# Kernel optimization log

Measured on AMD Instinct MI355X. Metric: run time of the kernel, lower is better.

The kernel has to match this reference:

```python
import jax, jax.numpy as jnp
import numpy as np

# irreps_in  = 128x0 + 64x1   (128 scalars, 64 vectors) -> dim 320
# irreps_out = 128x0 + 64x1 ; irreps_with_gates = (128+64)x0 + 64x1
B = 8192          # batch (nodes)
N0, N1 = 128, 64  # input multiplicities: scalars, vectors
NS, NV = 128, 64  # output scalars, gated vectors (NV gates appended to scalars)

_eps = np.zeros((3, 3, 3), np.float32)
_eps[0, 1, 2] = _eps[1, 2, 0] = _eps[2, 0, 1] = 1.0
_eps[0, 2, 1] = _eps[2, 1, 0] = _eps[1, 0, 2] = -1.0
EPS = jnp.asarray(_eps)  # Levi-Civita, used for the 1x1->1 CG path


def setup_inputs() -> dict:
    key = jax.random.key(0)
    ks = jax.random.split(key, 5)
    x = jax.random.normal(ks[0], (B, N0 + 3 * N1), jnp.float32)
    # fully-connected (uvw) path weights of the tensor square
    w000 = jax.random.normal(ks[1], (N0, N0, NS + NV), jnp.float32)
    w110 = jax.random.normal(ks[2], (N1, N1, NS + NV), jnp.float32)
    w011 = jax.random.normal(ks[3], (N0, N1, NV), jnp.float32)
    w111 = jax.random.normal(ks[4], (N1, N1, NV), jnp.float32)
    return {"x": x, "w000": w000, "w110": w110, "w011": w011, "w111": w111}


def reference(x, w000, w110, w011, w111):
    x0 = x[:, :N0]                        # [B, N0] scalars
    x1 = x[:, N0:].reshape(-1, N1, 3)     # [B, N1, 3] vectors

    inv_sqrt2 = 1.0 / np.sqrt(2.0)

    # ---- tensor square, scalar (l=0) outputs: NS scalars + NV gates ----
    s000 = jnp.einsum('bu,bv,uvw->bw', x0, x0, w000) * (1.0 / N0)
    dots = jnp.einsum('bui,bvi->buv', x1, x1) * (1.0 / np.sqrt(3.0))
    s110 = jnp.einsum('buv,uvw->bw', dots, w110) * (1.0 / N1)
    scalars = (s000 + s110) * inv_sqrt2   # [B, NS+NV], avg over 2 paths

    # ---- tensor square, vector (l=1) outputs: NV vectors ----
    v011 = jnp.einsum('bu,bvi,uvw->bwi', x0, x1, w011) * (1.0 / np.sqrt(N0 * N1))
    v111 = jnp.einsum('ijk,bui,bvj,uvw->bwk', EPS, x1, x1, w111) * (inv_sqrt2 / N1)
    vecs = (v011 + v111) * inv_sqrt2      # [B, NV, 3]

    # ---- e3nn.nn.Gate ----
    s_out = jax.nn.silu(scalars[:, :NS])            # act_scalars on true scalars
    g = jax.nn.sigmoid(scalars[:, NS:])             # act_gates on NV gate scalars
    v_out = vecs * g[:, :, None]                    # gate the non-scalar irreps

    return jnp.concatenate([s_out, v_out.reshape(v_out.shape[0], -1)], axis=1)
```

## Files before the change

### kernel.cpp

```cpp
#include <hip/hip_runtime.h>
#include <cstdint>

static constexpr int B_  = 8192;
static constexpr int NW_ = 192;

typedef __attribute__((ext_vector_type(8))) _Float16 h8v;
typedef __attribute__((ext_vector_type(2))) _Float16 h2v;
typedef __attribute__((ext_vector_type(4))) float f4v;
typedef __attribute__((ext_vector_type(2))) float f2v;
typedef __attribute__((ext_vector_type(4))) unsigned u4v;
typedef __attribute__((ext_vector_type(2))) unsigned u2v;

#define DI __device__ __forceinline__

DI h2v uh(unsigned u) { return __builtin_bit_cast(h2v, u); }
DI unsigned hu(h2v h) { return __builtin_bit_cast(unsigned, h); }
DI h2v hsplat(unsigned short bits) {
  _Float16 v = __builtin_bit_cast(_Float16, bits);
  h2v t; t.x = v; t.y = v; return t;
}
DI unsigned hpack(float lo, float hi) {
  h2v t; t.x = (_Float16)lo; t.y = (_Float16)hi;
  return __builtin_bit_cast(unsigned, t);
}
DI short f2h_bits(float f) { return __builtin_bit_cast(short, (_Float16)f); }

DI f4v mfma16h(h8v a, h8v b, f4v c) {
  return __builtin_amdgcn_mfma_f32_16x16x32_f16(a, b, c, 0, 0, 0);
}

static constexpr unsigned PK_BU0 = 606436u;
static constexpr unsigned PK_BV0 = 1030628u;
static constexpr unsigned PK_BU2 = 4u;
static constexpr unsigned PK_BV2 = 20u;
DI int tab2(unsigned pack, int blk) { return (int)((pack >> (2 * blk)) & 3u); }

__global__ void prep_all(const float* __restrict__ w000, const float* __restrict__ w110,
                         const float* __restrict__ w011, const float* __restrict__ w111,
                         short* __restrict__ wsc, short* __restrict__ wve) {
  __shared__ unsigned short T[32][200];
  const int t = threadIdx.x;
  const int bi = blockIdx.x;
  const float s000 = 1.0f / (128.0f * 1.41421356237f);
  const float s110 = 1.0f / (64.0f * 2.44948974968f);
  const float sv   = 1.0f / 128.0f;

  if (bi < 416) {
    const int s = bi;
    const float* W; int dim; float scale; int blk, ik, bu, bv;
    if (s < 320) {
      blk = s >> 5; ik = s & 31;
      bu = tab2(PK_BU0, blk); bv = tab2(PK_BV0, blk);
      W = w000; dim = 128; scale = s000;
    } else {
      int sp = s - 320; blk = sp >> 5; ik = sp & 31;
      bu = tab2(PK_BU2, blk); bv = tab2(PK_BV2, blk);
      W = w110; dim = 64; scale = s110;
    }
    const int u = bu * 32 + ik;
    const int v = t >> 3, l8 = t & 7;
    float a[24];
    const float* pA = W + ((size_t)(u * dim) + bv * 32 + v) * 192 + l8 * 24;
#pragma unroll
    for (int jj = 0; jj < 6; ++jj) {
      f4v x4 = *(const f4v*)(pA + jj * 4);
      a[jj * 4] = x4.x; a[jj * 4 + 1] = x4.y; a[jj * 4 + 2] = x4.z; a[jj * 4 + 3] = x4.w;
    }
    if (bu != bv) {
      const float* pB = W + ((size_t)((bv * 32 + v)) * dim + u) * 192 + l8 * 24;
#pragma unroll
      for (int jj = 0; jj < 6; ++jj) {
        f4v x4 = *(const f4v*)(pB + jj * 4);
        a[jj * 4] += x4.x; a[jj * 4 + 1] += x4.y; a[jj * 4 + 2] += x4.z; a[jj * 4 + 3] += x4.w;
      }
    }
    unsigned o[12];
#pragma unroll
    for (int i = 0; i < 12; ++i) o[i] = hpack(a[2 * i] * scale, a[2 * i + 1] * scale);
#pragma unroll
    for (int i = 0; i < 3; ++i)
      *(u4v*)(&T[v][l8 * 24 + i * 8]) = u4v{o[4 * i], o[4 * i + 1], o[4 * i + 2], o[4 * i + 3]};
    __syncthreads();
    short* dst = wsc + (size_t)s * 6144;
#pragma unroll
    for (int k = 0; k < 3; ++k) {
      const int unit = t * 3 + k;
      const int F = unit >> 6, lane = unit & 63;
      const int n = F * 16 + (lane & 15);
      const int vr = (lane >> 4) * 8;
      short oo[8];
#pragma unroll
      for (int j = 0; j < 8; ++j) oo[j] = (short)T[vr + j][n];
      *(h8v*)(dst + F * 512 + lane * 8) = *(h8v*)oo;
    }
  } else {
    const int s = bi - 416;
    if (s < 256) {
      const int k32 = t >> 3, l8 = t & 7;
      const float* p = w011 + ((size_t)(s * 32 + k32)) * 64 + l8 * 8;
      f4v x0_ = *(const f4v*)p, x1_ = *(const f4v*)(p + 4);
      u4v o{hpack(x0_.x * sv, x0_.y * sv), hpack(x0_.z * sv, x0_.w * sv),
            hpack(x1_.x * sv, x1_.y * sv), hpack(x1_.z * sv, x1_.w * sv)};
      *(u4v*)(&T[k32][l8 * 8]) = o;
    } else {
      const int sp = s - 256;
      const int blk = sp >> 5, ik = sp & 31;
      const int bu = tab2(PK_BU2, blk), bv = tab2(PK_BV2, blk);
      const int u = bu * 32 + ik;
      const int v = t >> 3, l8 = t & 7;
      float a[8];
      const float* pA = w111 + ((size_t)(u * 64) + bv * 32 + v) * 64 + l8 * 8;
      f4v x0_ = *(const f4v*)pA, x1_ = *(const f4v*)(pA + 4);
      a[0] = x0_.x; a[1] = x0_.y; a[2] = x0_.z; a[3] = x0_.w;
      a[4] = x1_.x; a[5] = x1_.y; a[6] = x1_.z; a[7] = x1_.w;
      if (bu != bv) {
        const float* pB = w111 + ((size_t)((bv * 32 + v)) * 64 + u) * 64 + l8 * 8;
        f4v y0 = *(const f4v*)pB, y1 = *(const f4v*)(pB + 4);
        a[0] -= y0.x; a[1] -= y0.y; a[2] -= y0.z; a[3] -= y0.w;
        a[4] -= y1.x; a[5] -= y1.y; a[6] -= y1.z; a[7] -= y1.w;
      }
      u4v o{hpack(a[0] * sv, a[1] * sv), hpack(a[2] * sv, a[3] * sv),
            hpack(a[4] * sv, a[5] * sv), hpack(a[6] * sv, a[7] * sv)};
      *(u4v*)(&T[v][l8 * 8]) = o;
    }
    __syncthreads();
    const int nf = t >> 6, lane = t & 63;
    const int n = nf * 16 + (lane & 15);
    const int vr = (lane >> 4) * 8;
    short oo[8];
#pragma unroll
    for (int j = 0; j < 8; ++j) oo[j] = (short)T[vr + j][n];
    *(h8v*)(wve + (size_t)s * 2048 + nf * 512 + lane * 8) = *(h8v*)oo;
  }
}

#define X0H_STRIDE 136
#define X1_STRIDE  200

DI void stage_x64w(const float* __restrict__ x, int b0,
                   unsigned short* X0H, unsigned short* X1) {
  const int t = threadIdx.x;
#pragma unroll
  for (int pass = 0; pass < 2; ++pass) {
    const int row = pass * 32 + (t >> 4), l16 = t & 15;
    const float* src = x + (size_t)(b0 + row) * 320;
    f4v v0 = *(const f4v*)(src + l16 * 8);
    f4v v1 = *(const f4v*)(src + l16 * 8 + 4);
    u4v o{hpack(v0.x, v0.y), hpack(v0.z, v0.w), hpack(v1.x, v1.y), hpack(v1.z, v1.w)};
    *(u4v*)(&X0H[row * X0H_STRIDE + l16 * 8]) = o;
    float buf[12];
    f4v a0 = *(const f4v*)(src + 128 + l16 * 12);
    f4v a1 = *(const f4v*)(src + 128 + l16 * 12 + 4);
    f4v a2 = *(const f4v*)(src + 128 + l16 * 12 + 8);
    buf[0] = a0.x; buf[1] = a0.y; buf[2] = a0.z; buf[3] = a0.w;
    buf[4] = a1.x; buf[5] = a1.y; buf[6] = a1.z; buf[7] = a1.w;
    buf[8] = a2.x; buf[9] = a2.y; buf[10] = a2.z; buf[11] = a2.w;
#pragma unroll
    for (int i = 0; i < 3; ++i) {
      u2v w2{hpack(buf[i], buf[3 + i]), hpack(buf[6 + i], buf[9 + i])};
      *(u2v*)(&X1[row * X1_STRIDE + i * 64 + l16 * 4]) = w2;
    }
  }
}

DI void loadB6(h8v* dst, const short* __restrict__ p) {
#pragma unroll
  for (int nf = 0; nf < 6; ++nf) dst[nf] = *(const h8v*)(p + nf * 512);
}
DI void loadB2(h8v* dst, const short* __restrict__ p) {
  dst[0] = *(const h8v*)p;
  dst[1] = *(const h8v*)(p + 512);
}

__global__ __launch_bounds__(512, 2)
void gemm_split(const float* __restrict__ x, const short* __restrict__ wsc,
                const short* __restrict__ wve,
                float* __restrict__ Psc, float* __restrict__ Pve) {
  __shared__ unsigned short X0H[64 * X0H_STRIDE];
  __shared__ unsigned short X1[64 * X1_STRIDE];
  const int xcd = blockIdx.x & 7;
  const int kb  = xcd >> 2;
  const int tile = (blockIdx.x >> 3) * 4 + (xcd & 3);
  const int b0 = tile * 64;

  stage_x64w(x, b0, X0H, X1);
  __syncthreads();

  const int t0 = threadIdx.x;
  const int w = t0 >> 6, lane = t0 & 63;
  const bool isvec = w >= 4;
  const int nh = w & 1, mr = (w >> 1) & 1;
  const int q = lane >> 4, r = lane & 15, q8 = q * 8;

  f4v acc[12];
#pragma unroll
  for (int i = 0; i < 12; ++i) acc[i] = f4v{0.f, 0.f, 0.f, 0.f};

  if (!isvec) {
    const unsigned short* x0f[2];
    const unsigned short* x1f[2];
#pragma unroll
    for (int f = 0; f < 2; ++f) {
      x0f[f] = &X0H[(mr * 32 + f * 16 + r) * X0H_STRIDE];
      x1f[f] = &X1[(mr * 32 + f * 16 + r) * X1_STRIDE];
    }

    {
      const int s0 = kb * 160;
      const short* wp = wsc + ((size_t)s0 * 12 + nh * 6) * 512 + lane * 8;
      u4v pv[2]; pv[0] = u4v{0, 0, 0, 0}; pv[1] = u4v{0, 0, 0, 0};
      int bu32 = 0;
      h8v b[4][6];
      loadB6(b[0], wp); loadB6(b[1], wp + 6144); loadB6(b[2], wp + 12288);
      for (int t4 = 0; t4 < 40; ++t4) {
#pragma unroll
        for (int uu = 0; uu < 4; ++uu) {
          const int t = t4 * 4 + uu;
          if (t < 157) loadB6(b[(uu + 3) & 3], wp + (size_t)(t + 3) * 6144);
          const int s = s0 + t;
          const int ik = s & 31;
          if (t == 0 || ik == 0) {
            const int blk = s >> 5;
            const int bv32 = tab2(PK_BV0, blk) * 32;
            bu32 = tab2(PK_BU0, blk) * 32;
            pv[0] = *(const u4v*)(x0f[0] + bv32 + q8);
            pv[1] = *(const u4v*)(x0f[1] + bv32 + q8);
          }
          h8v a[2];
#pragma unroll
          for (int f = 0; f < 2; ++f) {
            h2v xu = hsplat(x0f[f][bu32 + ik]);
            u4v pa;
#pragma unroll
            for (int m = 0; m < 4; ++m) pa[m] = hu(uh(pv[f][m]) * xu);
            a[f] = __builtin_bit_cast(h8v, pa);
          }
          __builtin_amdgcn_s_setprio(1);
#pragma unroll
          for (int nf = 0; nf < 6; ++nf)
#pragma unroll
            for (int f = 0; f < 2; ++f)
              acc[f * 6 + nf] = mfma16h(a[f], b[uu & 3][nf], acc[f * 6 + nf]);
          __builtin_amdgcn_s_setprio(0);
        }
      }
    }

    {
      const int sp0 = kb * 48;
      const short* wp = wsc + ((size_t)(320 + sp0) * 12 + nh * 6) * 512 + lane * 8;
      h8v b[4][6];
      loadB6(b[0], wp); loadB6(b[1], wp + 6144); loadB6(b[2], wp + 12288);
      for (int t4 = 0; t4 < 12; ++t4) {
#pragma unroll
        for (int uu = 0; uu < 4; ++uu) {
          const int t = t4 * 4 + uu;
          if (t < 45) loadB6(b[(uu + 3) & 3], wp + (size_t)(t + 3) * 6144);
          const int sp = sp0 + t;
          const int blk = sp >> 5, ik = sp & 31;
          const int bu32 = tab2(PK_BU2, blk) * 32;
          const int bv32 = tab2(PK_BV2, blk) * 32;
          h8v a[2];
#pragma unroll
          for (int f = 0; f < 2; ++f) {
            h2v us0 = hsplat(x1f[f][bu32 + ik]);
            h2v us1 = hsplat(x1f[f][64 + bu32 + ik]);
            h2v us2 = hsplat(x1f[f][128 + bu32 + ik]);
            u4v p0 = *(const u4v*)(x1f[f] + bv32 + q8);
            u4v p1 = *(const u4v*)(x1f[f] + 64 + bv32 + q8);
            u4v p2 = *(const u4v*)(x1f[f] + 128 + bv32 + q8);
            u4v pa;
#pragma unroll
            for (int m = 0; m < 4; ++m) {
              h2v sm = uh(p0[m]) * us0;
              sm = sm + uh(p1[m]) * us1;
              sm = sm + uh(p2[m]) * us2;
              pa[m] = hu(sm);
            }
            a[f] = __builtin_bit_cast(h8v, pa);
          }
          __builtin_amdgcn_s_setprio(1);
#pragma unroll
          for (int nf = 0; nf < 6; ++nf)
#pragma unroll
            for (int f = 0; f < 2; ++f)
              acc[f * 6 + nf] = mfma16h(a[f], b[uu & 3][nf], acc[f * 6 + nf]);
          __builtin_amdgcn_s_setprio(0);
        }
      }
    }

#pragma unroll
    for (int f = 0; f < 2; ++f)
#pragma unroll
      for (int nf = 0; nf < 6; ++nf) {
        const int n = (nh * 6 + nf) * 16 + r;
#pragma unroll
        for (int reg = 0; reg < 4; ++reg) {
          const int row = b0 + mr * 32 + f * 16 + q * 4 + reg;
          Psc[((size_t)kb * B_ + row) * NW_ + n] = acc[f * 6 + nf][reg];
        }
      }
  } else {
    const unsigned short* x0r[2];
    const unsigned short* x1r[2];
#pragma unroll
    for (int ff = 0; ff < 2; ++ff) {
      x0r[ff] = &X0H[(mr * 32 + ff * 16 + r) * X0H_STRIDE];
      x1r[ff] = &X1[(mr * 32 + ff * 16 + r) * X1_STRIDE];
    }

    {
      const int u0 = kb * 64;
      const short* wp = wve + (size_t)(u0 * 2) * 2048 + nh * 1024 + lane * 8;
      h8v b[4][2];
      loadB2(b[0], wp); loadB2(b[1], wp + 2048); loadB2(b[2], wp + 4096);
      for (int t4 = 0; t4 < 32; ++t4) {
#pragma unroll
        for (int uu = 0; uu < 4; ++uu) {
          const int t = t4 * 4 + uu;
          if (t < 125) loadB2(b[(uu + 3) & 3], wp + (size_t)(t + 3) * 2048);
          const int g = t >> 1, j = t & 1;
          const int vb = j * 32 + q8;
          h8v a[2][3];
#pragma unroll
          for (int ff = 0; ff < 2; ++ff) {
            h2v xu2 = hsplat(x0r[ff][u0 + g]);
#pragma unroll
            for (int i = 0; i < 3; ++i) {
              u4v p = *(const u4v*)(x1r[ff] + i * 64 + vb);
              u4v pa;
#pragma unroll
              for (int m = 0; m < 4; ++m) pa[m] = hu(uh(p[m]) * xu2);
              a[ff][i] = __builtin_bit_cast(h8v, pa);
            }
          }
          __builtin_amdgcn_s_setprio(1);
#pragma unroll
          for (int ip = 0; ip < 3; ++ip)
#pragma unroll
            for (int nfl = 0; nfl < 2; ++nfl)
#pragma unroll
              for (int ff = 0; ff < 2; ++ff)
                acc[(ff * 3 + ip) * 2 + nfl] =
                    mfma16h(a[ff][ip], b[uu & 3][nfl], acc[(ff * 3 + ip) * 2 + nfl]);
          __builtin_amdgcn_s_setprio(0);
        }
      }
    }

    {
      const int sp0 = kb * 48;
      const short* wp = wve + (size_t)(256 + sp0) * 2048 + nh * 1024 + lane * 8;
      h8v b[4][2];
      loadB2(b[0], wp); loadB2(b[1], wp + 2048); loadB2(b[2], wp + 4096);
      for (int t4 = 0; t4 < 12; ++t4) {
#pragma unroll
        for (int uu = 0; uu < 4; ++uu) {
          const int t = t4 * 4 + uu;
          if (t < 45) loadB2(b[(uu + 3) & 3], wp + (size_t)(t + 3) * 2048);
          const int sp = sp0 + t;
          const int blk = sp >> 5, ik = sp & 31;
          const int bu32 = tab2(PK_BU2, blk) * 32;
          const int bv32 = tab2(PK_BV2, blk) * 32;
          h8v a[2][3];
#pragma unroll
          for (int ff = 0; ff < 2; ++ff) {
            h2v us[3];
            u4v p[3];
#pragma unroll
            for (int i = 0; i < 3; ++i) {
              us[i] = hsplat(x1r[ff][i * 64 + bu32 + ik]);
              p[i] = *(const u4v*)(x1r[ff] + i * 64 + bv32 + q8);
            }
#pragma unroll
            for (int ip = 0; ip < 3; ++ip) {
              const int i1 = (ip + 1) % 3, i2 = (ip + 2) % 3;
              u4v pa;
#pragma unroll
              for (int m = 0; m < 4; ++m)
                pa[m] = hu(uh(p[i2][m]) * us[i1] - uh(p[i1][m]) * us[i2]);
              a[ff][ip] = __builtin_bit_cast(h8v, pa);
            }
          }
          __builtin_amdgcn_s_setprio(1);
#pragma unroll
          for (int ip = 0; ip < 3; ++ip)
#pragma unroll
            for (int nfl = 0; nfl < 2; ++nfl)
#pragma unroll
              for (int ff = 0; ff < 2; ++ff)
                acc[(ff * 3 + ip) * 2 + nfl] =
                    mfma16h(a[ff][ip], b[uu & 3][nfl], acc[(ff * 3 + ip) * 2 + nfl]);
          __builtin_amdgcn_s_setprio(0);
        }
      }
    }

#pragma unroll
    for (int ff = 0; ff < 2; ++ff)
#pragma unroll
      for (int ip = 0; ip < 3; ++ip)
#pragma unroll
        for (int nfl = 0; nfl < 2; ++nfl) {
          const int ai = (ff * 3 + ip) * 2 + nfl;
          const int n = (nh * 2 + nfl) * 16 + r;
#pragma unroll
          for (int reg = 0; reg < 4; ++reg) {
            const int row = b0 + mr * 32 + ff * 16 + q * 4 + reg;
            Pve[(((size_t)kb * 3 + ip) * B_ + row) * 64 + n] = acc[ai][reg];
          }
        }
  }
}

__global__ void reduce_ep(const float* __restrict__ Psc, const float* __restrict__ Pve,
                          float* __restrict__ out) {
  int t = blockIdx.x * blockDim.x + threadIdx.x;
  int b = t / NW_, c = t % NW_;
  float v = Psc[(size_t)b * NW_ + c] + Psc[(size_t)(B_ + b) * NW_ + c];
  float sg = 1.0f / (1.0f + __expf(-v));
  if (c < 128) {
    out[(size_t)b * 320 + c] = v * sg;
  } else {
    int w = c - 128;
#pragma unroll
    for (int i = 0; i < 3; ++i) {
      float vv = Pve[((size_t)i * B_ + b) * 64 + w] +
                 Pve[((size_t)(3 + i) * B_ + b) * 64 + w];
      out[(size_t)b * 320 + 128 + w * 3 + i] = vv * sg;
    }
  }
}

extern "C" void kernel_launch(void* const* d_in, const int* in_sizes, int n_in,
                              void* d_out, int out_size, void* d_ws, size_t ws_size,
                              hipStream_t stream) {
  const float* x    = (const float*)d_in[0];
  const float* w000 = (const float*)d_in[1];
  const float* w110 = (const float*)d_in[2];
  const float* w011 = (const float*)d_in[3];
  const float* w111 = (const float*)d_in[4];
  float* out = (float*)d_out;

  char* ws = (char*)d_ws;
  short* wsc = (short*)ws;
  short* wve = (short*)(ws + 5111808);
  float* Psc = (float*)(ws + 6553600);
  float* Pve = (float*)(ws + 19136512);

  prep_all  <<<768, 256, 0, stream>>>(w000, w110, w011, w111, wsc, wve);
  gemm_split<<<256, 512, 0, stream>>>(x, wsc, wve, Psc, Pve);
  reduce_ep <<<6144, 256, 0, stream>>>(Psc, Pve, out);
}
```

Before: 159.5 us.

## Split K across wave pairs with full M tile per wave, reduce via LDS

Each wave now covers all 64 rows of the tile and half of the K range, instead of 32 rows and the full K. Every B fragment loaded from global memory therefore feeds twice as many MFMAs, which halves per-wave weight traffic. The two K-halves are summed through a new 96KB shared-memory dump before the store. In exchange the accumulators double to 24 f4v per wave, which raises register pressure, and the large LDS buffer may reduce how many blocks fit per CU under launch_bounds(512,2). The vector paths also interleave A construction with the MFMAs.

```diff
diff --git a/kernel.cpp b/kernel.cpp
--- a/kernel.cpp
+++ b/kernel.cpp
@@ -178,6 +178,7 @@
                 float* __restrict__ Psc, float* __restrict__ Pve) {
   __shared__ unsigned short X0H[64 * X0H_STRIDE];
   __shared__ unsigned short X1[64 * X1_STRIDE];
+  __shared__ f4v dump[4][24][64];
   const int xcd = blockIdx.x & 7;
   const int kb  = xcd >> 2;
   const int tile = (blockIdx.x >> 3) * 4 + (xcd & 3);
@@ -189,46 +190,48 @@
   const int t0 = threadIdx.x;
   const int w = t0 >> 6, lane = t0 & 63;
   const bool isvec = w >= 4;
-  const int nh = w & 1, mr = (w >> 1) & 1;
+  const int nh = w & 1, kh = (w >> 1) & 1;
   const int q = lane >> 4, r = lane & 15, q8 = q * 8;
 
-  f4v acc[12];
-#pragma unroll
-  for (int i = 0; i < 12; ++i) acc[i] = f4v{0.f, 0.f, 0.f, 0.f};
+  f4v acc[24];
+#pragma unroll
+  for (int i = 0; i < 24; ++i) acc[i] = f4v{0.f, 0.f, 0.f, 0.f};
 
   if (!isvec) {
-    const unsigned short* x0f[2];
-    const unsigned short* x1f[2];
-#pragma unroll
-    for (int f = 0; f < 2; ++f) {
-      x0f[f] = &X0H[(mr * 32 + f * 16 + r) * X0H_STRIDE];
-      x1f[f] = &X1[(mr * 32 + f * 16 + r) * X1_STRIDE];
+    const unsigned short* x0f[4];
+    const unsigned short* x1f[4];
+#pragma unroll
+    for (int f = 0; f < 4; ++f) {
+      x0f[f] = &X0H[(f * 16 + r) * X0H_STRIDE];
+      x1f[f] = &X1[(f * 16 + r) * X1_STRIDE];
     }
 
     {
-      const int s0 = kb * 160;
+      const int s0 = kb * 160 + kh * 80;
       const short* wp = wsc + ((size_t)s0 * 12 + nh * 6) * 512 + lane * 8;
-      u4v pv[2]; pv[0] = u4v{0, 0, 0, 0}; pv[1] = u4v{0, 0, 0, 0};
+      u4v pv[4];
+#pragma unroll
+      for (int f = 0; f < 4; ++f) pv[f] = u4v{0, 0, 0, 0};
       int bu32 = 0;
       h8v b[4][6];
       loadB6(b[0], wp); loadB6(b[1], wp + 6144); loadB6(b[2], wp + 12288);
-      for (int t4 = 0; t4 < 40; ++t4) {
+      for (int t4 = 0; t4 < 20; ++t4) {
 #pragma unroll
         for (int uu = 0; uu < 4; ++uu) {
           const int t = t4 * 4 + uu;
-          if (t < 157) loadB6(b[(uu + 3) & 3], wp + (size_t)(t + 3) * 6144);
+          if (t < 77) loadB6(b[(uu + 3) & 3], wp + (size_t)(t + 3) * 6144);
           const int s = s0 + t;
           const int ik = s & 31;
           if (t == 0 || ik == 0) {
             const int blk = s >> 5;
             const int bv32 = tab2(PK_BV0, blk) * 32;
             bu32 = tab2(PK_BU0, blk) * 32;
-            pv[0] = *(const u4v*)(x0f[0] + bv32 + q8);
-            pv[1] = *(const u4v*)(x0f[1] + bv32 + q8);
-          }
-          h8v a[2];
-#pragma unroll
-          for (int f = 0; f < 2; ++f) {
+#pragma unroll
+            for (int f = 0; f < 4; ++f) pv[f] = *(const u4v*)(x0f[f] + bv32 + q8);
+          }
+          h8v a[4];
+#pragma unroll
+          for (int f = 0; f < 4; ++f) {
             h2v xu = hsplat(x0f[f][bu32 + ik]);
             u4v pa;
 #pragma unroll
@@ -239,7 +242,7 @@
 #pragma unroll
           for (int nf = 0; nf < 6; ++nf)
 #pragma unroll
-            for (int f = 0; f < 2; ++f)
+            for (int f = 0; f < 4; ++f)
               acc[f * 6 + nf] = mfma16h(a[f], b[uu & 3][nf], acc[f * 6 + nf]);
           __builtin_amdgcn_s_setprio(0);
         }
@@ -247,22 +250,22 @@
     }
 
     {
-      const int sp0 = kb * 48;
+      const int sp0 = kb * 48 + kh * 24;
       const short* wp = wsc + ((size_t)(320 + sp0) * 12 + nh * 6) * 512 + lane * 8;
       h8v b[4][6];
       loadB6(b[0], wp); loadB6(b[1], wp + 6144); loadB6(b[2], wp + 12288);
-      for (int t4 = 0; t4 < 12; ++t4) {
+      for (int t4 = 0; t4 < 6; ++t4) {
 #pragma unroll
         for (int uu = 0; uu < 4; ++uu) {
           const int t = t4 * 4 + uu;
-          if (t < 45) loadB6(b[(uu + 3) & 3], wp + (size_t)(t + 3) * 6144);
+          if (t < 21) loadB6(b[(uu + 3) & 3], wp + (size_t)(t + 3) * 6144);
           const int sp = sp0 + t;
           const int blk = sp >> 5, ik = sp & 31;
           const int bu32 = tab2(PK_BU2, blk) * 32;
           const int bv32 = tab2(PK_BV2, blk) * 32;
-          h8v a[2];
-#pragma unroll
-          for (int f = 0; f < 2; ++f) {
+          h8v a[4];
+#pragma unroll
+          for (int f = 0; f < 4; ++f) {
             h2v us0 = hsplat(x1f[f][bu32 + ik]);
             h2v us1 = hsplat(x1f[f][64 + bu32 + ik]);
             h2v us2 = hsplat(x1f[f][128 + bu32 + ik]);
@@ -283,89 +286,75 @@
 #pragma unroll
           for (int nf = 0; nf < 6; ++nf)
 #pragma unroll
-            for (int f = 0; f < 2; ++f)
+            for (int f = 0; f < 4; ++f)
               acc[f * 6 + nf] = mfma16h(a[f], b[uu & 3][nf], acc[f * 6 + nf]);
           __builtin_amdgcn_s_setprio(0);
         }
       }
     }
-
-#pragma unroll
-    for (int f = 0; f < 2; ++f)
-#pragma unroll
-      for (int nf = 0; nf < 6; ++nf) {
-        const int n = (nh * 6 + nf) * 16 + r;
-#pragma unroll
-        for (int reg = 0; reg < 4; ++reg) {
-          const int row = b0 + mr * 32 + f * 16 + q * 4 + reg;
-          Psc[((size_t)kb * B_ + row) * NW_ + n] = acc[f * 6 + nf][reg];
-        }
-      }
   } else {
-    const unsigned short* x0r[2];
-    const unsigned short* x1r[2];
-#pragma unroll
-    for (int ff = 0; ff < 2; ++ff) {
-      x0r[ff] = &X0H[(mr * 32 + ff * 16 + r) * X0H_STRIDE];
-      x1r[ff] = &X1[(mr * 32 + ff * 16 + r) * X1_STRIDE];
+    const unsigned short* x0r[4];
+    const unsigned short* x1r[4];
+#pragma unroll
+    for (int ff = 0; ff < 4; ++ff) {
+      x0r[ff] = &X0H[(ff * 16 + r) * X0H_STRIDE];
+      x1r[ff] = &X1[(ff * 16 + r) * X1_STRIDE];
     }
 
     {
-      const int u0 = kb * 64;
+      const int u0 = kb * 64 + kh * 32;
       const short* wp = wve + (size_t)(u0 * 2) * 2048 + nh * 1024 + lane * 8;
       h8v b[4][2];
       loadB2(b[0], wp); loadB2(b[1], wp + 2048); loadB2(b[2], wp + 4096);
-      for (int t4 = 0; t4 < 32; ++t4) {
+      for (int t4 = 0; t4 < 16; ++t4) {
 #pragma unroll
         for (int uu = 0; uu < 4; ++uu) {
           const int t = t4 * 4 + uu;
-          if (t < 125) loadB2(b[(uu + 3) & 3], wp + (size_t)(t + 3) * 2048);
+          if (t < 61) loadB2(b[(uu + 3) & 3], wp + (size_t)(t + 3) * 2048);
           const int g = t >> 1, j = t & 1;
           const int vb = j * 32 + q8;
-          h8v a[2][3];
-#pragma unroll
-          for (int ff = 0; ff < 2; ++ff) {
+          __builtin_amdgcn_s_setprio(1);
+#pragma unroll
+          for (int ff = 0; ff < 4; ++ff) {
             h2v xu2 = hsplat(x0r[ff][u0 + g]);
+            h8v a[3];
 #pragma unroll
             for (int i = 0; i < 3; ++i) {
               u4v p = *(const u4v*)(x1r[ff] + i * 64 + vb);
               u4v pa;
 #pragma unroll
               for (int m = 0; m < 4; ++m) pa[m] = hu(uh(p[m]) * xu2);
-              a[ff][i] = __builtin_bit_cast(h8v, pa);
+              a[i] = __builtin_bit_cast(h8v, pa);
             }
-          }
-          __builtin_amdgcn_s_setprio(1);
-#pragma unroll
-          for (int ip = 0; ip < 3; ++ip)
-#pragma unroll
-            for (int nfl = 0; nfl < 2; ++nfl)
-#pragma unroll
-              for (int ff = 0; ff < 2; ++ff)
-                acc[(ff * 3 + ip) * 2 + nfl] =
-                    mfma16h(a[ff][ip], b[uu & 3][nfl], acc[(ff * 3 + ip) * 2 + nfl]);
+#pragma unroll
+            for (int ip = 0; ip < 3; ++ip)
+#pragma unroll
+              for (int nfl = 0; nfl < 2; ++nfl)
+                acc[ff * 6 + ip * 2 + nfl] =
+                    mfma16h(a[ip], b[uu & 3][nfl], acc[ff * 6 + ip * 2 + nfl]);
+          }
           __builtin_amdgcn_s_setprio(0);
         }
       }
     }
 
     {
-      const int sp0 = kb * 48;
+      const int sp0 = kb * 48 + kh * 24;
       const short* wp = wve + (size_t)(256 + sp0) * 2048 + nh * 1024 + lane * 8;
       h8v b[4][2];
       loadB2(b[0], wp); loadB2(b[1], wp + 2048); loadB2(b[2], wp + 4096);
-      for (int t4 = 0; t4 < 12; ++t4) {
+      for (int t4 = 0; t4 < 6; ++t4) {
 #pragma unroll
         for (int uu = 0; uu < 4; ++uu) {
           const int t = t4 * 4 + uu;
-          if (t < 45) loadB2(b[(uu + 3) & 3], wp + (size_t)(t + 3) * 2048);
+          if (t < 21) loadB2(b[(uu + 3) & 3], wp + (size_t)(t + 3) * 2048);
           const int sp = sp0 + t;
           const int blk = sp >> 5, ik = sp & 31;
           const int bu32 = tab2(PK_BU2, blk) * 32;
           const int bv32 = tab2(PK_BV2, blk) * 32;
-          h8v a[2][3];
-#pragma unroll
-          for (int ff = 0; ff < 2; ++ff) {
+          __builtin_amdgcn_s_setprio(1);
+#pragma unroll
+          for (int ff = 0; ff < 4; ++ff) {
             h2v us[3];
             u4v p[3];
 #pragma unroll
@@ -380,35 +369,54 @@
 #pragma unroll
               for (int m = 0; m < 4; ++m)
                 pa[m] = hu(uh(p[i2][m]) * us[i1] - uh(p[i1][m]) * us[i2]);
-              a[ff][ip] = __builtin_bit_cast(h8v, pa);
+              h8v av = __builtin_bit_cast(h8v, pa);
+#pragma unroll
+              for (int nfl = 0; nfl < 2; ++nfl)
+                acc[ff * 6 + ip * 2 + nfl] =
+                    mfma16h(av, b[uu & 3][nfl], acc[ff * 6 + ip * 2 + nfl]);
             }
           }
-          __builtin_amdgcn_s_setprio(1);
-#pragma unroll
-          for (int ip = 0; ip < 3; ++ip)
-#pragma unroll
-            for (int nfl = 0; nfl < 2; ++nfl)
-#pragma unroll
-              for (int ff = 0; ff < 2; ++ff)
-                acc[(ff * 3 + ip) * 2 + nfl] =
-                    mfma16h(a[ff][ip], b[uu & 3][nfl], acc[(ff * 3 + ip) * 2 + nfl]);
           __builtin_amdgcn_s_setprio(0);
         }
       }
     }
-
-#pragma unroll
-    for (int ff = 0; ff < 2; ++ff)
+  }
+
+  const int slot = (isvec ? 2 : 0) + nh;
+  if (kh == 1) {
+#pragma unroll
+    for (int i = 0; i < 24; ++i) dump[slot][i][lane] = acc[i];
+  }
+  __syncthreads();
+
+  if (kh == 0 && !isvec) {
+#pragma unroll
+    for (int f = 0; f < 4; ++f)
+#pragma unroll
+      for (int nf = 0; nf < 6; ++nf) {
+        f4v v = acc[f * 6 + nf] + dump[slot][f * 6 + nf][lane];
+        const int n = (nh * 6 + nf) * 16 + r;
+#pragma unroll
+        for (int reg = 0; reg < 4; ++reg) {
+          const int row = b0 + f * 16 + q * 4 + reg;
+          Psc[((size_t)kb * B_ + row) * NW_ + n] = v[reg];
+        }
+      }
+  }
+  if (kh == 0 && isvec) {
+#pragma unroll
+    for (int ff = 0; ff < 4; ++ff)
 #pragma unroll
       for (int ip = 0; ip < 3; ++ip)
 #pragma unroll
         for (int nfl = 0; nfl < 2; ++nfl) {
-          const int ai = (ff * 3 + ip) * 2 + nfl;
+          const int ai = ff * 6 + ip * 2 + nfl;
+          f4v v = acc[ai] + dump[slot][ai][lane];
           const int n = (nh * 2 + nfl) * 16 + r;
 #pragma unroll
           for (int reg = 0; reg < 4; ++reg) {
-            const int row = b0 + mr * 32 + ff * 16 + q * 4 + reg;
-            Pve[(((size_t)kb * 3 + ip) * B_ + row) * 64 + n] = acc[ai][reg];
+            const int row = b0 + ff * 16 + q * 4 + reg;
+            Pve[(((size_t)kb * 3 + ip) * B_ + row) * 64 + n] = v[reg];
           }
         }
   }
```

Result: slower. 177.5 us (+11.3%).
